# Kernel optimization log

Hardware: AMD Instinct MI355X
Metric: run time of the kernel (lower is better)

## Reference

```python
import jax, jax.numpy as jnp
import numpy as np

T = 4096          # num tokens
HID = 2048        # hidden_size
HQ = 32           # num q heads
HKV = 8           # num kv heads
G = HQ // HKV     # GQA group size
D = 128           # head_dim (q/k)
DV = 96           # v_head_dim
W = 512           # sliding window (= query block size)
THETA = 1e6
Q_SIZE, K_SIZE, V_SIZE = HQ * D, HKV * D, HKV * DV


def setup_inputs() -> dict:
    key = jax.random.key(0)
    k1, k2, k3, k4 = jax.random.split(key, 4)
    positions = jnp.arange(T, dtype=jnp.int32)
    hidden_states = jax.random.normal(k1, (T, HID), dtype=jnp.float32)
    qkv_w = jax.random.normal(k2, (Q_SIZE + K_SIZE + V_SIZE, HID), dtype=jnp.float32) * (HID ** -0.5)
    o_w = jax.random.normal(k3, (HID, HQ * DV), dtype=jnp.float32) * ((HQ * DV) ** -0.5)
    sink_bias = jax.random.normal(k4, (HQ,), dtype=jnp.float32)
    return {"positions": positions, "hidden_states": hidden_states,
            "qkv_w": qkv_w, "o_w": o_w, "sink_bias": sink_bias}


def _rope(x, positions):
    # neox-style rotate-half RoPE on full head_dim (partial_rotary_factor=1.0)
    half = D // 2
    inv_freq = 1.0 / (THETA ** (jnp.arange(0, half, dtype=jnp.float32) / half))
    ang = positions.astype(jnp.float32)[:, None] * inv_freq[None, :]   # [T, D/2]
    cos = jnp.cos(ang)[:, None, :]
    sin = jnp.sin(ang)[:, None, :]
    x1, x2 = x[..., :half], x[..., half:]
    return jnp.concatenate([x1 * cos - x2 * sin, x2 * cos + x1 * sin], axis=-1)


def _swa_with_sink(q, k, v, sink_bias):
    # q: [T, HKV, G, D], k: [T, HKV, D], v: [T, HKV, DV]
    nb = T // W
    scale = D ** -0.5
    qb = q.reshape(nb, W, HKV, G, D)
    # per query block i, keys/values from global span [(i-1)*W, (i+1)*W)
    k_pad = jnp.pad(k, ((W, 0), (0, 0), (0, 0)))
    v_pad = jnp.pad(v, ((W, 0), (0, 0), (0, 0)))
    idx = jnp.arange(nb)[:, None] * W + jnp.arange(2 * W)[None, :]     # [nb, 2W]
    k_ext = k_pad[idx]                                                 # [nb, 2W, HKV, D]
    v_ext = v_pad[idx]                                                 # [nb, 2W, HKV, DV]
    # mask: rel = t - j in [0, W); exclude left-pad keys (key_pos < 0)
    r = jnp.arange(W)[:, None]
    c = jnp.arange(2 * W)[None, :]
    rel = W + r - c                                                    # [W, 2W]
    key_pos = (jnp.arange(nb)[:, None, None] - 1) * W + c[None]        # [nb, W(1), 2W]
    mask = (rel >= 0) & (rel < W) & (key_pos >= 0)                     # [nb, W, 2W]
    scores = jnp.einsum('nrkgd,nckd->nkgrc', qb, k_ext) * scale        # [nb,HKV,G,W,2W]
    scores = jnp.where(mask[:, None, None, :, :], scores, -jnp.inf)
    sink = jnp.broadcast_to(sink_bias.reshape(HKV, G)[None, :, :, None, None],
                            (nb, HKV, G, W, 1))
    logits = jnp.concatenate([scores, sink], axis=-1)                  # [...,2W+1]
    p = jax.nn.softmax(logits, axis=-1)[..., :-1]                      # drop sink column
    out = jnp.einsum('nkgrc,nckd->nrkgd', p, v_ext)                    # [nb,W,HKV,G,DV]
    return out.reshape(T, HQ * DV)


def reference(positions, hidden_states, qkv_w, o_w, sink_bias):
    qkv = hidden_states @ qkv_w.T                                      # [T, Q+K+V]
    q, k, v = jnp.split(qkv, [Q_SIZE, Q_SIZE + K_SIZE], axis=-1)
    q = q.reshape(T, HQ, D)
    k = k.reshape(T, HKV, D)
    v = v.reshape(T, HKV, DV)
    q = _rope(q, positions).reshape(T, HKV, G, D)
    k = _rope(k, positions)
    attn = _swa_with_sink(q, k, v, sink_bias)                          # [T, HQ*DV]
    return attn @ o_w.T                                                # [T, HID]
```

## Files before the change

### kernel.cpp

```cpp
#include <hip/hip_runtime.h>
#include <hip/hip_bf16.h>
#include <stdint.h>

#define T_SEQ 4096
#define HIDDEN 2048
#define NQH 32
#define NKVH 8
#define DH 128
#define DVH 96
#define WWIN 512
#define QKVN 5888
#define KOFF 4096
#define VOFF 5120
#define ATTN 3072
#define QSCALE 0.08838834764831845f

typedef uint16_t u16;
typedef uint32_t u32;
typedef __bf16 bfrag8 __attribute__((ext_vector_type(8)));
typedef float f32x4v __attribute__((ext_vector_type(4)));

__device__ __forceinline__ u16 f2bf(float x) {
  u32 u = __float_as_uint(x);
  return (u16)((u + 0x7fffu + ((u >> 16) & 1u)) >> 16);
}
__device__ __forceinline__ float bf2f(u16 v) { return __uint_as_float(((u32)v) << 16); }

__global__ void cvt_kernel(const float* __restrict__ in, u16* __restrict__ out, int n4) {
  int i = blockIdx.x * blockDim.x + threadIdx.x;
  int st = gridDim.x * blockDim.x;
  for (; i < n4; i += st) {
    float4 v = ((const float4*)in)[i];
    ushort4 o;
    o.x = f2bf(v.x); o.y = f2bf(v.y); o.z = f2bf(v.z); o.w = f2bf(v.w);
    ((ushort4*)out)[i] = o;
  }
}

template<int WN, int OUT_F32>
__global__ __launch_bounds__(512, 2) void gemm_pipe(const u16* __restrict__ A,
                                                    const u16* __restrict__ B,
                                                    void* __restrict__ Cp,
                                                    int M, int N, int K, int nbm) {
  constexpr int BN = WN * 64;
  constexpr int WM = 8 / WN;
  constexpr int MF = 16 / WM;
  constexpr int ASZ = 8192;
  constexpr int BSZ = BN * 32;
  constexpr int BUFSZ = ASZ + BSZ;
  constexpr int AIN = 2;
  constexpr int BIN = (WN == 4) ? 2 : 1;
  constexpr int LPT = AIN + BIN;

  extern __shared__ u16 lds[];

  const int tid = threadIdx.x;
  const int w = tid >> 6, lane = tid & 63;
  const int wr = w / WN, wc = w % WN;
  const int fr = lane & 15, kg = lane >> 4;

  const int nwg = gridDim.x;
  int bid = (int)blockIdx.x;
  if ((nwg & 7) == 0) bid = (bid & 7) * (nwg >> 3) + (bid >> 3);
  const int bm = (bid % nbm) * 256;
  const int bn = (bid / nbm) * BN;

  const int NT = K >> 5;

  f32x4v acc[MF][4];
#pragma unroll
  for (int m = 0; m < MF; m++)
#pragma unroll
    for (int n = 0; n < 4; n++) acc[m][n] = {0.f, 0.f, 0.f, 0.f};

  auto stageA = [&](int t) {
    u16* dst = lds + (t % 3) * BUFSZ;
#pragma unroll
    for (int i = 0; i < AIN; i++) {
      int D = (w * AIN + i) * 1024 + lane * 16;
      int srow = D >> 7;
      int Dx = D ^ ((srow & 7) << 4);
      int c = (Dx >> 1) & 63;
      int m = 2 * srow + (c >> 5);
      int k = c & 31;
      const u16* src = A + (size_t)(bm + m) * K + (t << 5) + k;
      __builtin_amdgcn_global_load_lds((const __attribute__((address_space(1))) u32*)src,
                                       (__attribute__((address_space(3))) u32*)((char*)dst + D),
                                       16, 0, 0);
    }
  };
  auto stageB = [&](int t) {
    u16* dst = lds + (t % 3) * BUFSZ + ASZ;
#pragma unroll
    for (int i = 0; i < BIN; i++) {
      int D = (w * BIN + i) * 1024 + lane * 16;
      int srow = D >> 7;
      int Dx = D ^ ((srow & 7) << 4);
      int c = (Dx >> 1) & 63;
      int m = 2 * srow + (c >> 5);
      int k = c & 31;
      const u16* src = B + (size_t)(bn + m) * K + (t << 5) + k;
      __builtin_amdgcn_global_load_lds((const __attribute__((address_space(1))) u32*)src,
                                       (__attribute__((address_space(3))) u32*)((char*)dst + D),
                                       16, 0, 0);
    }
  };

  stageA(0); stageB(0);
  stageA(1); stageB(1);

  for (int t = 0; t < NT; ++t) {
    const u16* At = lds + (t % 3) * BUFSZ;
    const u16* Bt = At + ASZ;
    if (t + 1 < NT) asm volatile("s_waitcnt vmcnt(%0)" :: "n"(LPT));
    else            asm volatile("s_waitcnt vmcnt(0)");
    asm volatile("s_barrier" ::: "memory");

    bfrag8 bfr[4];
#pragma unroll
    for (int n = 0; n < 4; n++) {
      int nr = wc * 64 + n * 16 + fr;
      int byt = (((nr >> 1) << 7) + ((nr & 1) << 6) + (kg << 4)) ^ (((nr >> 1) & 7) << 4);
      bfr[n] = *(const bfrag8*)((const char*)Bt + byt);
    }
    bfrag8 afr[MF / 2];
#pragma unroll
    for (int m = 0; m < MF / 2; m++) {
      int mr = wr * (MF * 16) + m * 16 + fr;
      int byt = (((mr >> 1) << 7) + ((mr & 1) << 6) + (kg << 4)) ^ (((mr >> 1) & 7) << 4);
      afr[m] = *(const bfrag8*)((const char*)At + byt);
    }
    if (t + 2 < NT) stageA(t + 2);
    __builtin_amdgcn_s_setprio(1);
#pragma unroll
    for (int m = 0; m < MF / 2; m++)
#pragma unroll
      for (int n = 0; n < 4; n++)
        acc[m][n] = __builtin_amdgcn_mfma_f32_16x16x32_bf16(afr[m], bfr[n], acc[m][n], 0, 0, 0);
    __builtin_amdgcn_s_setprio(0);
    asm volatile("s_barrier" ::: "memory");

    bfrag8 afr2[MF / 2];
#pragma unroll
    for (int m = 0; m < MF / 2; m++) {
      int mr = wr * (MF * 16) + (m + MF / 2) * 16 + fr;
      int byt = (((mr >> 1) << 7) + ((mr & 1) << 6) + (kg << 4)) ^ (((mr >> 1) & 7) << 4);
      afr2[m] = *(const bfrag8*)((const char*)At + byt);
    }
    if (t + 2 < NT) stageB(t + 2);
    __builtin_amdgcn_s_setprio(1);
#pragma unroll
    for (int m = 0; m < MF / 2; m++)
#pragma unroll
      for (int n = 0; n < 4; n++)
        acc[m + MF / 2][n] = __builtin_amdgcn_mfma_f32_16x16x32_bf16(afr2[m], bfr[n], acc[m + MF / 2][n], 0, 0, 0);
    __builtin_amdgcn_s_setprio(0);
  }

  const int rb = bm + wr * (MF * 16);
  const int cb = bn + wc * 64;
#pragma unroll
  for (int m = 0; m < MF; m++)
#pragma unroll
    for (int n = 0; n < 4; n++) {
      size_t base = (size_t)(rb + m * 16 + kg * 4) * N + cb + n * 16 + fr;
#pragma unroll
      for (int r = 0; r < 4; r++) {
        if (OUT_F32) ((float*)Cp)[base + (size_t)r * N] = acc[m][n][r];
        else         ((u16*)Cp)[base + (size_t)r * N] = f2bf(acc[m][n][r]);
      }
    }
}

template<int OUT_F32>
__global__ __launch_bounds__(256) void gemm_nt(const u16* __restrict__ A,
                                               const u16* __restrict__ B,
                                               void* __restrict__ Cp,
                                               int M, int N, int K) {
  __shared__ u16 Asm[128 * 32];
  __shared__ u16 Bsm[128 * 32];
  const int tid = threadIdx.x;
  const int wv = tid >> 6, lane = tid & 63;
  const int bm = blockIdx.x * 128, bn = blockIdx.y * 128;
  const int wm = (wv >> 1) * 64, wn = (wv & 1) * 64;
  const int srow = lane >> 2;
  const int scol = (lane & 3) * 8;
  const int fr = lane & 15, fk = (lane >> 4) * 8;
  f32x4v acc[4][4];
#pragma unroll
  for (int i = 0; i < 4; i++)
#pragma unroll
    for (int j = 0; j < 4; j++) acc[i][j] = {0.f, 0.f, 0.f, 0.f};

  for (int kt = 0; kt < K; kt += 32) {
    __syncthreads();
#pragma unroll
    for (int c = 0; c < 2; c++) {
      const int ci = wv * 2 + c;
      const u16* ga = A + (size_t)(bm + ci * 16 + srow) * K + kt + scol;
      const u16* gb = B + (size_t)(bn + ci * 16 + srow) * K + kt + scol;
      __builtin_amdgcn_global_load_lds((const __attribute__((address_space(1))) u32*)ga,
                                       (__attribute__((address_space(3))) u32*)(Asm + ci * 512),
                                       16, 0, 0);
      __builtin_amdgcn_global_load_lds((const __attribute__((address_space(1))) u32*)gb,
                                       (__attribute__((address_space(3))) u32*)(Bsm + ci * 512),
                                       16, 0, 0);
    }
    __syncthreads();
    bfrag8 af[4], bf[4];
#pragma unroll
    for (int i = 0; i < 4; i++) af[i] = *(const bfrag8*)(Asm + (wm + i * 16 + fr) * 32 + fk);
#pragma unroll
    for (int j = 0; j < 4; j++) bf[j] = *(const bfrag8*)(Bsm + (wn + j * 16 + fr) * 32 + fk);
#pragma unroll
    for (int i = 0; i < 4; i++)
#pragma unroll
      for (int j = 0; j < 4; j++)
        acc[i][j] = __builtin_amdgcn_mfma_f32_16x16x32_bf16(af[i], bf[j], acc[i][j], 0, 0, 0);
  }
  const int orow = (lane >> 4) * 4, ocol = lane & 15;
#pragma unroll
  for (int i = 0; i < 4; i++)
#pragma unroll
    for (int j = 0; j < 4; j++) {
      size_t base = (size_t)(bm + wm + i * 16 + orow) * N + (size_t)(bn + wn + j * 16 + ocol);
#pragma unroll
      for (int r = 0; r < 4; r++) {
        if (OUT_F32) ((float*)Cp)[base + (size_t)r * N] = acc[i][j][r];
        else         ((u16*)Cp)[base + (size_t)r * N] = f2bf(acc[i][j][r]);
      }
    }
}

__global__ void rope_kernel(u16* __restrict__ qkv, const int* __restrict__ pos) {
  int gid = blockIdx.x * 256 + threadIdx.x;
  int d = gid & 63;
  int r = gid >> 6;
  int hh = r % 40;
  int t = r / 40;
  if (t >= T_SEQ) return;
  int off = (hh < 32) ? hh * 128 : KOFF + (hh - 32) * 128;
  u16* p = qkv + (size_t)t * QKVN + off + d;
  float x1 = bf2f(p[0]);
  float x2 = bf2f(p[64]);
  float inv_freq = exp2f(-(float)d * 0.3114307588956852f);
  float ang = (float)pos[t] * inv_freq;
  float c = cosf(ang), s = sinf(ang);
  float y1 = x1 * c - x2 * s;
  float y2 = x2 * c + x1 * s;
  if (hh < 32) { y1 *= QSCALE; y2 *= QSCALE; }
  p[0] = f2bf(y1);
  p[64] = f2bf(y2);
}

__global__ __launch_bounds__(256) void vt_kernel(const u16* __restrict__ qkv,
                                                 u16* __restrict__ vt) {
  __shared__ u16 tile[64][100];
  const int t0 = blockIdx.x * 64;
  const int hk = blockIdx.y;
  const int tid = threadIdx.x;
#pragma unroll
  for (int i = 0; i < 3; i++) {
    int idx = i * 256 + tid;
    int row = idx / 12, ch = idx % 12;
    const u16* g = qkv + (size_t)(t0 + row) * QKVN + VOFF + hk * DVH + ch * 8;
    uint2 a = *(const uint2*)g;
    uint2 b = *(const uint2*)(g + 4);
    *(uint2*)&tile[row][ch * 8] = a;
    *(uint2*)&tile[row][ch * 8 + 4] = b;
  }
  __syncthreads();
#pragma unroll
  for (int i = 0; i < 3; i++) {
    int idx = i * 256 + tid;
    int dv = idx >> 3, tc = (idx & 7) * 8;
    union { uint4 v4; u16 s[8]; } o;
#pragma unroll
    for (int j = 0; j < 8; j++) o.s[j] = tile[tc + j][dv];
    *(uint4*)(vt + (((size_t)(hk * 96 + dv)) << 12) + t0 + tc) = o.v4;
  }
}

__global__ __launch_bounds__(256, 2) void attn_mfma(const u16* __restrict__ qkv,
                                                    const u16* __restrict__ vt,
                                                    const float* __restrict__ sink_bias,
                                                    u16* __restrict__ attn_out) {
  __shared__ u16 k_lds[64 * 128];
  __shared__ u16 v_lds[96 * 64];
  __shared__ u16 p_lds[4][2048];

  const int tid = threadIdx.x;
  const int wv = tid >> 6;
  const int lane = tid & 63;
  const int g = lane >> 4;
  const int c = lane & 15;
  const int t0 = blockIdx.x * 32;
  const int hk = blockIdx.y;
  const int h = hk * 4 + wv;

  bfrag8 qf[2][4];
#pragma unroll
  for (int m = 0; m < 2; m++)
#pragma unroll
    for (int kf = 0; kf < 4; kf++)
      qf[m][kf] = *(const bfrag8*)(qkv + (size_t)(t0 + m * 16 + c) * QKVN + h * DH + kf * 32 + g * 8);

  f32x4v acc_o[2][6];
#pragma unroll
  for (int m = 0; m < 2; m++)
#pragma unroll
    for (int n = 0; n < 6; n++) acc_o[m][n] = {0.f, 0.f, 0.f, 0.f};

  const float sb = sink_bias[h];
  float m_run[2][4], l_run[2][4];
#pragma unroll
  for (int m = 0; m < 2; m++)
#pragma unroll
    for (int r = 0; r < 4; r++) { m_run[m][r] = sb; l_run[m][r] = 1.0f; }

  int cb0 = t0 - (WWIN - 1);
  cb0 = (cb0 < 0) ? 0 : (cb0 & ~63);

  for (int cb = cb0; cb < t0 + 32; cb += 64) {
    __syncthreads();
#pragma unroll
    for (int it = 0; it < 4; it++) {
      int dest = it * 4096 + tid * 16;
      int row = dest >> 8;
      int src = dest ^ ((row & 7) << 4);
      const u16* gp = qkv + (size_t)(cb + row) * QKVN + KOFF + hk * DH + ((src & 255) >> 1);
      __builtin_amdgcn_global_load_lds((const __attribute__((address_space(1))) u32*)gp,
                                       (__attribute__((address_space(3))) u32*)((char*)k_lds + dest),
                                       16, 0, 0);
    }
#pragma unroll
    for (int it = 0; it < 3; it++) {
      int dest = it * 4096 + tid * 16;
      int row = dest >> 7;
      int src = dest ^ ((row & 7) << 4);
      const u16* gp = vt + (((size_t)(hk * 96 + row)) << 12) + cb + ((src & 127) >> 1);
      __builtin_amdgcn_global_load_lds((const __attribute__((address_space(1))) u32*)gp,
                                       (__attribute__((address_space(3))) u32*)((char*)v_lds + dest),
                                       16, 0, 0);
    }
    __syncthreads();

    f32x4v s[2][4];
#pragma unroll
    for (int m = 0; m < 2; m++)
#pragma unroll
      for (int n = 0; n < 4; n++) s[m][n] = {0.f, 0.f, 0.f, 0.f};
#pragma unroll
    for (int kf = 0; kf < 4; kf++) {
      bfrag8 kb[4];
#pragma unroll
      for (int n = 0; n < 4; n++) {
        int key = n * 16 + c;
        int byt = ((key << 8) + (kf << 6) + (g << 4)) ^ ((key & 7) << 4);
        kb[n] = *(const bfrag8*)((const char*)k_lds + byt);
      }
#pragma unroll
      for (int m = 0; m < 2; m++)
#pragma unroll
        for (int n = 0; n < 4; n++)
          s[m][n] = __builtin_amdgcn_mfma_f32_16x16x32_bf16(qf[m][kf], kb[n], s[m][n], 0, 0, 0);
    }

    if ((cb + 63 > t0) || (cb + WWIN < t0 + 32)) {
#pragma unroll
      for (int m = 0; m < 2; m++)
#pragma unroll
        for (int n = 0; n < 4; n++)
#pragma unroll
          for (int r = 0; r < 4; r++) {
            int rel = (t0 + m * 16 + g * 4 + r) - (cb + n * 16 + c);
            if (!(rel >= 0 && rel < WWIN)) s[m][n][r] = -3.0e38f;
          }
    }

    float corr[2][4];
#pragma unroll
    for (int m = 0; m < 2; m++)
#pragma unroll
      for (int r = 0; r < 4; r++) {
        float v0 = fmaxf(fmaxf(s[m][0][r], s[m][1][r]), fmaxf(s[m][2][r], s[m][3][r]));
        v0 = fmaxf(v0, __shfl_xor(v0, 1));
        v0 = fmaxf(v0, __shfl_xor(v0, 2));
        v0 = fmaxf(v0, __shfl_xor(v0, 4));
        v0 = fmaxf(v0, __shfl_xor(v0, 8));
        float mn = fmaxf(m_run[m][r], v0);
        corr[m][r] = __expf(m_run[m][r] - mn);
        m_run[m][r] = mn;
        float p0 = __expf(s[m][0][r] - mn);
        float p1 = __expf(s[m][1][r] - mn);
        float p2 = __expf(s[m][2][r] - mn);
        float p3 = __expf(s[m][3][r] - mn);
        s[m][0][r] = p0; s[m][1][r] = p1; s[m][2][r] = p2; s[m][3][r] = p3;
        float rs = p0 + p1 + p2 + p3;
        rs += __shfl_xor(rs, 1);
        rs += __shfl_xor(rs, 2);
        rs += __shfl_xor(rs, 4);
        rs += __shfl_xor(rs, 8);
        l_run[m][r] = l_run[m][r] * corr[m][r] + rs;
      }
#pragma unroll
    for (int m = 0; m < 2; m++)
#pragma unroll
      for (int n = 0; n < 6; n++)
#pragma unroll
      for (int r = 0; r < 4; r++) acc_o[m][n][r] *= corr[m][r];

#pragma unroll
    for (int m = 0; m < 2; m++)
#pragma unroll
      for (int n = 0; n < 4; n++) {
        u32 lo = (u32)f2bf(s[m][n][0]) | ((u32)f2bf(s[m][n][1]) << 16);
        u32 hi = (u32)f2bf(s[m][n][2]) | ((u32)f2bf(s[m][n][3]) << 16);
        int byt = ((m * 2 + (n >> 1)) << 10) | (g << 3) | ((c & 3) << 5) |
                  (((c >> 2) & 1) << 9) | ((((n & 1) * 2) + (c >> 3)) << 7);
        uint2 u; u.x = lo; u.y = hi;
        *(uint2*)((char*)&p_lds[wv][0] + byt) = u;
      }

#pragma unroll
    for (int ks = 0; ks < 2; ks++) {
      bfrag8 pa[2];
#pragma unroll
      for (int m = 0; m < 2; m++) {
        union { bfrag8 v; u16 s16[8]; } u;
#pragma unroll
        for (int j = 0; j < 4; j++) {
          int e = ((m * 2 + ks) << 9) + c + j * 16 + g * 64;
          u.s16[j] = p_lds[wv][e];
          u.s16[4 + j] = p_lds[wv][e + 256];
        }
        pa[m] = u.v;
      }
#pragma unroll
      for (int n = 0; n < 6; n++) {
        int dv = n * 16 + c;
        int byt = ((dv << 7) + (ks << 6) + (g << 4)) ^ ((dv & 7) << 4);
        bfrag8 vb = *(const bfrag8*)((const char*)v_lds + byt);
#pragma unroll
        for (int m = 0; m < 2; m++)
          acc_o[m][n] = __builtin_amdgcn_mfma_f32_16x16x32_bf16(pa[m], vb, acc_o[m][n], 0, 0, 0);
      }
    }
  }

#pragma unroll
  for (int m = 0; m < 2; m++) {
    float inv[4];
#pragma unroll
    for (int r = 0; r < 4; r++) inv[r] = 1.0f / l_run[m][r];
#pragma unroll
    for (int n = 0; n < 6; n++)
#pragma unroll
      for (int r = 0; r < 4; r++) {
        int tq = t0 + m * 16 + g * 4 + r;
        attn_out[(size_t)tq * ATTN + h * DVH + n * 16 + c] = f2bf(acc_o[m][n][r] * inv[r]);
      }
  }
}

extern "C" void kernel_launch(void* const* d_in, const int* in_sizes, int n_in,
                              void* d_out, int out_size, void* d_ws, size_t ws_size,
                              hipStream_t stream) {
  const int* positions = (const int*)d_in[0];
  const float* hidden = (const float*)d_in[1];
  const float* qkv_w = (const float*)d_in[2];
  const float* o_w = (const float*)d_in[3];
  const float* sink = (const float*)d_in[4];
  char* ws = (char*)d_ws;

  u16* hs_bf   = (u16*)(ws + 0);
  u16* w1_bf   = (u16*)(ws + 16777216);
  u16* attn_bf = (u16*)(ws + 0);
  u16* vt_buf  = (u16*)(ws + 25165824);
  u16* w2_bf   = (u16*)(ws + 40894464);
  u16* qkv_bf  = (u16*)(ws + 53477376);

  bool pipeOk =
    (hipFuncSetAttribute((const void*)&gemm_pipe<4, 0>,
                         hipFuncAttributeMaxDynamicSharedMemorySize, 98304) == hipSuccess) &&
    (hipFuncSetAttribute((const void*)&gemm_pipe<2, 1>,
                         hipFuncAttributeMaxDynamicSharedMemorySize, 73728) == hipSuccess);

  cvt_kernel<<<dim3(1024), dim3(256), 0, stream>>>(hidden, hs_bf, 8388608 / 4);
  cvt_kernel<<<dim3(1024), dim3(256), 0, stream>>>(qkv_w, w1_bf, 12058624 / 4);
  cvt_kernel<<<dim3(1024), dim3(256), 0, stream>>>(o_w, w2_bf, 6291456 / 4);

  if (pipeOk)
    gemm_pipe<4, 0><<<dim3(368), dim3(512), 98304, stream>>>(hs_bf, w1_bf, (void*)qkv_bf,
                                                             T_SEQ, QKVN, HIDDEN, 16);
  else
    gemm_nt<0><<<dim3(32, 46), dim3(256), 0, stream>>>(hs_bf, w1_bf, (void*)qkv_bf,
                                                       T_SEQ, QKVN, HIDDEN);

  rope_kernel<<<dim3(40960), dim3(256), 0, stream>>>(qkv_bf, positions);
  vt_kernel<<<dim3(T_SEQ / 64, NKVH), dim3(256), 0, stream>>>(qkv_bf, vt_buf);
  attn_mfma<<<dim3(T_SEQ / 32, NKVH), dim3(256), 0, stream>>>(qkv_bf, vt_buf, sink, attn_bf);

  if (pipeOk)
    gemm_pipe<2, 1><<<dim3(256), dim3(512), 73728, stream>>>(attn_bf, w2_bf, d_out,
                                                             T_SEQ, HIDDEN, ATTN, 16);
  else
    gemm_nt<1><<<dim3(32, 16), dim3(256), 0, stream>>>(attn_bf, w2_bf, d_out,
                                                       T_SEQ, HIDDEN, ATTN);
}
```

Baseline: 322.8 us.

## Add 256x256-tile ping-pong GEMM for QKV projection with split-phase MFMA scheduling

Adds a new bf16 GEMM kernel for the QKV projection. It uses 256x256 tiles with a 64-wide K step, double-buffered LDS (128KB) filled by direct global-to-LDS loads with XOR swizzle, and splits each K step into four MFMA phases interleaved with barriers and priority hints. The aim is to overlap global loads with compute and raise data reuse compared with the previous 256-wide-N pipeline. The risks are the large LDS footprint, which limits occupancy, and the many barriers per iteration.

```diff
diff --git a/kernel.cpp b/kernel.cpp
--- a/kernel.cpp
+++ b/kernel.cpp
@@ -35,6 +35,172 @@
     o.x = f2bf(v.x); o.y = f2bf(v.y); o.z = f2bf(v.z); o.w = f2bf(v.w);
     ((ushort4*)out)[i] = o;
   }
+}
+
+__global__ __launch_bounds__(512, 2) void gemm_8p(const u16* __restrict__ A,
+                                                  const u16* __restrict__ B,
+                                                  u16* __restrict__ C,
+                                                  int M, int N, int K, int nbm) {
+  extern __shared__ u16 lds[];
+  const int tid = threadIdx.x;
+  const int w = tid >> 6, lane = tid & 63;
+  const int wr = w >> 2, wc = w & 3;
+  const int fr = lane & 15, kg = lane >> 4;
+
+  const int nwg = gridDim.x;
+  int bid = (int)blockIdx.x;
+  if ((nwg & 7) == 0) bid = (bid & 7) * (nwg >> 3) + (bid >> 3);
+  const int bm = (bid % nbm) * 256;
+  const int bn = (bid / nbm) * 256;
+  const int NT = K >> 6;
+
+  f32x4v acc[8][4];
+#pragma unroll
+  for (int m = 0; m < 8; m++)
+#pragma unroll
+    for (int n = 0; n < 4; n++) acc[m][n] = {0.f, 0.f, 0.f, 0.f};
+
+  auto stageHalf = [&](const u16* rowbase, int kt, u16* dst) {
+#pragma unroll
+    for (int i = 0; i < 2; i++) {
+      int D = (i * 512 + tid) * 16;
+      int r = D >> 7;
+      int kb = (D ^ ((r & 7) << 4)) & 127;
+      const u16* gp = rowbase + (size_t)r * K + kt + (kb >> 1);
+      __builtin_amdgcn_global_load_lds((const __attribute__((address_space(1))) u32*)gp,
+                                       (__attribute__((address_space(3))) u32*)((char*)dst + D),
+                                       16, 0, 0);
+    }
+  };
+
+  const u16* Arow0 = A + (size_t)bm * K;
+  const u16* Arow1 = A + (size_t)(bm + 128) * K;
+  const u16* Brow0 = B + (size_t)bn * K;
+  const u16* Brow1 = B + (size_t)(bn + 128) * K;
+
+  stageHalf(Arow0, 0, lds);
+  stageHalf(Arow1, 0, lds + 8192);
+  stageHalf(Brow0, 0, lds + 16384);
+  stageHalf(Brow1, 0, lds + 24576);
+
+  const int bcol = (wc & 1) * 64;
+
+  for (int t = 0; t < NT; ++t) {
+    u16* buf = lds + (t & 1) * 32768;
+    u16* nbuf = lds + ((t + 1) & 1) * 32768;
+    const u16* Ah = buf + wr * 8192;
+    const u16* Bh = buf + 16384 + (wc >> 1) * 8192;
+
+    bfrag8 ar[4][2], br[4][2];
+
+    if (t + 1 < NT) {
+      stageHalf(Arow0, (t + 1) << 6, nbuf);
+      stageHalf(Arow1, (t + 1) << 6, nbuf + 8192);
+      asm volatile("s_waitcnt vmcnt(4)");
+    } else {
+      asm volatile("s_waitcnt vmcnt(0)");
+    }
+    asm volatile("s_barrier" ::: "memory");
+#pragma unroll
+    for (int rb = 0; rb < 4; rb++)
+#pragma unroll
+      for (int ks = 0; ks < 2; ks++) {
+        int row = rb * 16 + fr;
+        int byt = ((row << 7) | (ks << 6) | (kg << 4)) ^ ((row & 7) << 4);
+        ar[rb][ks] = *(const bfrag8*)((const char*)Ah + byt);
+      }
+#pragma unroll
+    for (int nb = 0; nb < 2; nb++)
+#pragma unroll
+      for (int ks = 0; ks < 2; ks++) {
+        int col = bcol + nb * 16 + fr;
+        int byt = ((col << 7) | (ks << 6) | (kg << 4)) ^ ((col & 7) << 4);
+        br[nb][ks] = *(const bfrag8*)((const char*)Bh + byt);
+      }
+    asm volatile("s_waitcnt lgkmcnt(0)" ::: "memory");
+    __builtin_amdgcn_sched_barrier(0);
+    __builtin_amdgcn_s_setprio(1);
+#pragma unroll
+    for (int rb = 0; rb < 4; rb++)
+#pragma unroll
+      for (int nb = 0; nb < 2; nb++)
+#pragma unroll
+        for (int ks = 0; ks < 2; ks++)
+          acc[rb][nb] = __builtin_amdgcn_mfma_f32_16x16x32_bf16(ar[rb][ks], br[nb][ks], acc[rb][nb], 0, 0, 0);
+    __builtin_amdgcn_s_setprio(0);
+    asm volatile("s_barrier" ::: "memory");
+
+#pragma unroll
+    for (int nb = 2; nb < 4; nb++)
+#pragma unroll
+      for (int ks = 0; ks < 2; ks++) {
+        int col = bcol + nb * 16 + fr;
+        int byt = ((col << 7) | (ks << 6) | (kg << 4)) ^ ((col & 7) << 4);
+        br[nb][ks] = *(const bfrag8*)((const char*)Bh + byt);
+      }
+    if (t + 1 < NT) {
+      stageHalf(Brow0, (t + 1) << 6, nbuf + 16384);
+      stageHalf(Brow1, (t + 1) << 6, nbuf + 24576);
+    }
+    asm volatile("s_barrier" ::: "memory");
+    asm volatile("s_waitcnt lgkmcnt(0)" ::: "memory");
+    __builtin_amdgcn_sched_barrier(0);
+    __builtin_amdgcn_s_setprio(1);
+#pragma unroll
+    for (int rb = 0; rb < 4; rb++)
+#pragma unroll
+      for (int nb = 2; nb < 4; nb++)
+#pragma unroll
+        for (int ks = 0; ks < 2; ks++)
+          acc[rb][nb] = __builtin_amdgcn_mfma_f32_16x16x32_bf16(ar[rb][ks], br[nb][ks], acc[rb][nb], 0, 0, 0);
+    __builtin_amdgcn_s_setprio(0);
+    asm volatile("s_barrier" ::: "memory");
+
+#pragma unroll
+    for (int rb = 0; rb < 4; rb++)
+#pragma unroll
+      for (int ks = 0; ks < 2; ks++) {
+        int row = 64 + rb * 16 + fr;
+        int byt = ((row << 7) | (ks << 6) | (kg << 4)) ^ ((row & 7) << 4);
+        ar[rb][ks] = *(const bfrag8*)((const char*)Ah + byt);
+      }
+    asm volatile("s_barrier" ::: "memory");
+    asm volatile("s_waitcnt lgkmcnt(0)" ::: "memory");
+    __builtin_amdgcn_sched_barrier(0);
+    __builtin_amdgcn_s_setprio(1);
+#pragma unroll
+    for (int rb = 0; rb < 4; rb++)
+#pragma unroll
+      for (int nb = 0; nb < 2; nb++)
+#pragma unroll
+        for (int ks = 0; ks < 2; ks++)
+          acc[4 + rb][nb] = __builtin_amdgcn_mfma_f32_16x16x32_bf16(ar[rb][ks], br[nb][ks], acc[4 + rb][nb], 0, 0, 0);
+    __builtin_amdgcn_s_setprio(0);
+    asm volatile("s_barrier" ::: "memory");
+
+    __builtin_amdgcn_s_setprio(1);
+#pragma unroll
+    for (int rb = 0; rb < 4; rb++)
+#pragma unroll
+      for (int nb = 2; nb < 4; nb++)
+#pragma unroll
+        for (int ks = 0; ks < 2; ks++)
+          acc[4 + rb][nb] = __builtin_amdgcn_mfma_f32_16x16x32_bf16(ar[rb][ks], br[nb][ks], acc[4 + rb][nb], 0, 0, 0);
+    __builtin_amdgcn_s_setprio(0);
+    asm volatile("s_barrier" ::: "memory");
+  }
+
+  const int rb0 = bm + wr * 128;
+  const int cb0 = bn + wc * 64;
+#pragma unroll
+  for (int m = 0; m < 8; m++)
+#pragma unroll
+    for (int n = 0; n < 4; n++) {
+      size_t base = (size_t)(rb0 + m * 16 + kg * 4) * N + cb0 + n * 16 + fr;
+#pragma unroll
+      for (int r = 0; r < 4; r++)
+        C[base + (size_t)r * N] = f2bf(acc[m][n][r]);
+    }
 }
 
 template<int WN, int OUT_F32>
@@ -480,19 +646,18 @@
   u16* w2_bf   = (u16*)(ws + 40894464);
   u16* qkv_bf  = (u16*)(ws + 53477376);
 
-  bool pipeOk =
-    (hipFuncSetAttribute((const void*)&gemm_pipe<4, 0>,
-                         hipFuncAttributeMaxDynamicSharedMemorySize, 98304) == hipSuccess) &&
-    (hipFuncSetAttribute((const void*)&gemm_pipe<2, 1>,
-                         hipFuncAttributeMaxDynamicSharedMemorySize, 73728) == hipSuccess);
+  bool p1Ok = (hipFuncSetAttribute((const void*)&gemm_8p,
+                 hipFuncAttributeMaxDynamicSharedMemorySize, 131072) == hipSuccess);
+  bool p2Ok = (hipFuncSetAttribute((const void*)&gemm_pipe<2, 1>,
+                 hipFuncAttributeMaxDynamicSharedMemorySize, 73728) == hipSuccess);
 
   cvt_kernel<<<dim3(1024), dim3(256), 0, stream>>>(hidden, hs_bf, 8388608 / 4);
   cvt_kernel<<<dim3(1024), dim3(256), 0, stream>>>(qkv_w, w1_bf, 12058624 / 4);
   cvt_kernel<<<dim3(1024), dim3(256), 0, stream>>>(o_w, w2_bf, 6291456 / 4);
 
-  if (pipeOk)
-    gemm_pipe<4, 0><<<dim3(368), dim3(512), 98304, stream>>>(hs_bf, w1_bf, (void*)qkv_bf,
-                                                             T_SEQ, QKVN, HIDDEN, 16);
+  if (p1Ok)
+    gemm_8p<<<dim3(368), dim3(512), 131072, stream>>>(hs_bf, w1_bf, qkv_bf,
+                                                      T_SEQ, QKVN, HIDDEN, 16);
   else
     gemm_nt<0><<<dim3(32, 46), dim3(256), 0, stream>>>(hs_bf, w1_bf, (void*)qkv_bf,
                                                        T_SEQ, QKVN, HIDDEN);
@@ -501,7 +666,7 @@
   vt_kernel<<<dim3(T_SEQ / 64, NKVH), dim3(256), 0, stream>>>(qkv_bf, vt_buf);
   attn_mfma<<<dim3(T_SEQ / 32, NKVH), dim3(256), 0, stream>>>(qkv_bf, vt_buf, sink, attn_bf);
 
-  if (pipeOk)
+  if (p2Ok)
     gemm_pipe<2, 1><<<dim3(256), dim3(512), 73728, stream>>>(attn_bf, w2_bf, d_out,
                                                              T_SEQ, HIDDEN, ATTN, 16);
   else
```

Result: no change. 321.3 us (-0.5%).
